# Optimization experiments

Hardware: AMD Instinct MI355X
Metric: run time of the kernel (lower is better)

Reference implementation:

```python
import jax, jax.numpy as jnp
import numpy as np

B, N = 8, 4096
DL = DR = DO = R = 256
SP = 3  # spatial tensor index dimension


def setup_inputs() -> dict:
    key = jax.random.key(0)
    k1, k2, k3, k4, k5 = jax.random.split(key, 5)
    x_l = jax.random.normal(k1, (B, N, DL, SP), dtype=jnp.float32)
    x_r = jax.random.normal(k2, (B, N, DR, SP), dtype=jnp.float32)
    # TensLinear self_init: normal with std = fan_in**-0.5
    W_l = jax.random.normal(k3, (R, DL), dtype=jnp.float32) * DL ** (-0.5)
    W_r = jax.random.normal(k4, (R, DR), dtype=jnp.float32) * DR ** (-0.5)
    W_o = jax.random.normal(k5, (DO, R), dtype=jnp.float32) * R ** (-0.5)
    return {"x_l": x_l, "x_r": x_r, "W_l": W_l, "W_r": W_r, "W_o": W_o}


def reference(x_l, x_r, W_l, W_r, W_o):
    # lin_l / lin_r: channel mixing into shared rank dim (tensor indices untouched)
    xl = jnp.einsum('OI,bnIi->bnOi', W_l, x_l)          # [B,N,R,3]
    xr = jnp.einsum('OI,bnIj->bnOj', W_r, x_r)          # [B,N,R,3]
    # inds_l=1, inds_r=1, inds_o=2 => contracts=0: outer product '...i,...j->...ij'
    xo = jnp.einsum('bnri,bnrj->bnrij', xl, xr)          # [B,N,R,3,3]
    # lin_o: mix rank -> dim_o
    return jnp.einsum('OI,bnIij->bnOij', W_o, xo)        # [B,N,DO,3,3]
```

## Files before the change

### kernel.cpp

```cpp
#include <hip/hip_runtime.h>

typedef short bf16x8 __attribute__((ext_vector_type(8)));
typedef float f32x4 __attribute__((ext_vector_type(4)));

__device__ inline unsigned short f2bf(float f) {
    union { float f; unsigned u; } v; v.f = f;
    unsigned u = v.u;
    u += 0x7fffu + ((u >> 16) & 1u);
    return (unsigned short)(u >> 16);
}

#define KPAD 264

__global__ void prep_weights(const float* __restrict__ wl,
                             const float* __restrict__ wr,
                             const float* __restrict__ wo,
                             unsigned short* __restrict__ wsw) {
    int idx = blockIdx.x * 256 + threadIdx.x;
    int w    = idx >> 16;
    int e    = idx & 65535;
    int jj   = e & 7;
    int lane = (e >> 3) & 63;
    int kmt  = e >> 9;
    int ks   = kmt & 7;
    int mt   = kmt >> 3;
    int row = mt * 16 + (lane & 15);
    int col = ks * 32 + (lane >> 4) * 8 + jj;
    const float* src = (w == 0) ? wl : (w == 1) ? wr : wo;
    wsw[idx] = f2bf(src[row * 256 + col]);
}

__global__ __launch_bounds__(512, 4) void fused_kernel(
    const float* __restrict__ xl_g, const float* __restrict__ xr_g,
    const unsigned short* __restrict__ wsw, float* __restrict__ out) {

    __shared__ __align__(16) unsigned short lds[38016];

    const int tid  = threadIdx.x;
    const int blk  = blockIdx.x;
    const int wave = tid >> 6;
    const int lane = tid & 63;
    const int q    = lane >> 4;
    const int l15  = lane & 15;

    const float* srcs[2] = { xl_g + (size_t)blk * 12288, xr_g + (size_t)blk * 12288 };
    for (int a = 0; a < 2; ++a) {
        const float4* s4 = (const float4*)srcs[a];
        unsigned short* dst = lds + a * 12672;
        #pragma unroll
        for (int it = 0; it < 6; ++it) {
            int g4 = it * 512 + tid;
            float4 v = s4[g4];
            int g = g4 * 4;
            int tok = g / 768;
            int m0 = g - tok * 768;
            float vv[4] = {v.x, v.y, v.z, v.w};
            #pragma unroll
            for (int e = 0; e < 4; ++e) {
                int mm = m0 + e;
                int I = mm / 3;
                int i = mm - I * 3;
                dst[(i * 16 + tok) * KPAD + I] = f2bf(vv[e]);
            }
        }
    }
    __syncthreads();

    const bf16x8* wlf = (const bf16x8*)(wsw);
    const bf16x8* wrf = (const bf16x8*)(wsw + 65536);
    const bf16x8* wof = (const bf16x8*)(wsw + 131072);

    f32x4 accL[2][3] = {};
    f32x4 accR[2][3] = {};

    #pragma unroll
    for (int k = 0; k < 8; ++k) {
        const int koff = k * 32 + q * 8;
        bf16x8 bl[3], br[3];
        #pragma unroll
        for (int nt = 0; nt < 3; ++nt) {
            bl[nt] = *(const bf16x8*)&lds[(nt * 16 + l15) * KPAD + koff];
            br[nt] = *(const bf16x8*)&lds[12672 + (nt * 16 + l15) * KPAD + koff];
        }
        #pragma unroll
        for (int m = 0; m < 2; ++m) {
            const int mt = wave * 2 + m;
            bf16x8 al = wlf[(mt * 8 + k) * 64 + lane];
            bf16x8 ar = wrf[(mt * 8 + k) * 64 + lane];
            #pragma unroll
            for (int nt = 0; nt < 3; ++nt) {
                accL[m][nt] = __builtin_amdgcn_mfma_f32_16x16x32_bf16(al, bl[nt], accL[m][nt], 0, 0, 0);
                accR[m][nt] = __builtin_amdgcn_mfma_f32_16x16x32_bf16(ar, br[nt], accR[m][nt], 0, 0, 0);
            }
        }
    }
    __syncthreads();

    #pragma unroll
    for (int m = 0; m < 2; ++m) {
        const int mt = wave * 2 + m;
        const int r0 = mt * 16 + q * 4;
        #pragma unroll
        for (int i = 0; i < 3; ++i) {
            #pragma unroll
            for (int j = 0; j < 3; ++j) {
                const int c = (i * 3 + j) * 16 + l15;
                unsigned short h[4];
                #pragma unroll
                for (int reg = 0; reg < 4; ++reg)
                    h[reg] = f2bf(accL[m][i][reg] * accR[m][j][reg]);
                uint2 pk;
                pk.x = (unsigned)h[0] | ((unsigned)h[1] << 16);
                pk.y = (unsigned)h[2] | ((unsigned)h[3] << 16);
                *(uint2*)&lds[c * KPAD + r0] = pk;
            }
        }
    }
    __syncthreads();

    const size_t tokbase = ((size_t)blk * 16 + l15) * 2304;
    #pragma unroll
    for (int pass = 0; pass < 2; ++pass) {
        const int p0 = pass ? 5 : 0;
        const int np = pass ? 4 : 5;
        f32x4 accO[2][5] = {};
        #pragma unroll
        for (int k = 0; k < 8; ++k) {
            const int koff = k * 32 + q * 8;
            bf16x8 pf[5];
            #pragma unroll
            for (int p = 0; p < np; ++p)
                pf[p] = *(const bf16x8*)&lds[((p0 + p) * 16 + l15) * KPAD + koff];
            #pragma unroll
            for (int m = 0; m < 2; ++m) {
                const int mt = wave * 2 + m;
                bf16x8 ao = wof[(mt * 8 + k) * 64 + lane];
                #pragma unroll
                for (int p = 0; p < np; ++p)
                    accO[m][p] = __builtin_amdgcn_mfma_f32_16x16x32_bf16(ao, pf[p], accO[m][p], 0, 0, 0);
            }
        }
        #pragma unroll
        for (int m = 0; m < 2; ++m) {
            const int mt = wave * 2 + m;
            #pragma unroll
            for (int reg = 0; reg < 4; ++reg) {
                const int o = mt * 16 + q * 4 + reg;
                float* dst = out + tokbase + o * 9 + p0;
                #pragma unroll
                for (int p = 0; p < np; ++p)
                    dst[p] = accO[m][p][reg];
            }
        }
    }
}

extern "C" void kernel_launch(void* const* d_in, const int* in_sizes, int n_in,
                              void* d_out, int out_size, void* d_ws, size_t ws_size,
                              hipStream_t stream) {
    const float* xl = (const float*)d_in[0];
    const float* xr = (const float*)d_in[1];
    const float* wl = (const float*)d_in[2];
    const float* wr = (const float*)d_in[3];
    const float* wo = (const float*)d_in[4];
    float* out = (float*)d_out;
    unsigned short* wsw = (unsigned short*)d_ws;

    prep_weights<<<768, 256, 0, stream>>>(wl, wr, wo, wsw);
    fused_kernel<<<2048, 512, 0, stream>>>(xl, xr, wsw, out);
}
```

Before: 534.1 us.

## Stage output tiles through LDS for coalesced float4 global stores

The final W_o GEMM now keeps both pass accumulators live and writes results into a per-wave LDS staging area, then writes contiguous float4 chunks per token to global memory. Previously each lane scattered scalar stores with a stride of 9 floats, which coalesces poorly for an output that dominates memory traffic. In exchange it raises register pressure, since all 9 accumulator tiles are live at once, and adds extra barriers and LDS traffic.

```diff
diff --git a/kernel.cpp b/kernel.cpp
--- a/kernel.cpp
+++ b/kernel.cpp
@@ -118,40 +118,65 @@
     }
     __syncthreads();
 
-    const size_t tokbase = ((size_t)blk * 16 + l15) * 2304;
+    f32x4 accA[2][5] = {};
+    f32x4 accB[2][4] = {};
     #pragma unroll
-    for (int pass = 0; pass < 2; ++pass) {
-        const int p0 = pass ? 5 : 0;
-        const int np = pass ? 4 : 5;
-        f32x4 accO[2][5] = {};
+    for (int k = 0; k < 8; ++k) {
+        const int koff = k * 32 + q * 8;
+        bf16x8 pf[5];
         #pragma unroll
-        for (int k = 0; k < 8; ++k) {
-            const int koff = k * 32 + q * 8;
-            bf16x8 pf[5];
-            #pragma unroll
-            for (int p = 0; p < np; ++p)
-                pf[p] = *(const bf16x8*)&lds[((p0 + p) * 16 + l15) * KPAD + koff];
-            #pragma unroll
-            for (int m = 0; m < 2; ++m) {
-                const int mt = wave * 2 + m;
-                bf16x8 ao = wof[(mt * 8 + k) * 64 + lane];
-                #pragma unroll
-                for (int p = 0; p < np; ++p)
-                    accO[m][p] = __builtin_amdgcn_mfma_f32_16x16x32_bf16(ao, pf[p], accO[m][p], 0, 0, 0);
-            }
-        }
+        for (int p = 0; p < 5; ++p)
+            pf[p] = *(const bf16x8*)&lds[(p * 16 + l15) * KPAD + koff];
         #pragma unroll
         for (int m = 0; m < 2; ++m) {
             const int mt = wave * 2 + m;
+            bf16x8 ao = wof[(mt * 8 + k) * 64 + lane];
             #pragma unroll
-            for (int reg = 0; reg < 4; ++reg) {
-                const int o = mt * 16 + q * 4 + reg;
-                float* dst = out + tokbase + o * 9 + p0;
-                #pragma unroll
-                for (int p = 0; p < np; ++p)
-                    dst[p] = accO[m][p][reg];
+            for (int p = 0; p < 5; ++p)
+                accA[m][p] = __builtin_amdgcn_mfma_f32_16x16x32_bf16(ao, pf[p], accA[m][p], 0, 0, 0);
+        }
+    }
+    #pragma unroll
+    for (int k = 0; k < 8; ++k) {
+        const int koff = k * 32 + q * 8;
+        bf16x8 pf[4];
+        #pragma unroll
+        for (int p = 0; p < 4; ++p)
+            pf[p] = *(const bf16x8*)&lds[((5 + p) * 16 + l15) * KPAD + koff];
+        #pragma unroll
+        for (int m = 0; m < 2; ++m) {
+            const int mt = wave * 2 + m;
+            bf16x8 ao = wof[(mt * 8 + k) * 64 + lane];
+            #pragma unroll
+            for (int p = 0; p < 4; ++p)
+                accB[m][p] = __builtin_amdgcn_mfma_f32_16x16x32_bf16(ao, pf[p], accB[m][p], 0, 0, 0);
+        }
+    }
+    __syncthreads();
+
+    float* sf = (float*)(lds + wave * 4736);
+    const int tok = lane >> 2, sub = lane & 3;
+    #pragma unroll
+    for (int m = 0; m < 2; ++m) {
+        const int mt = wave * 2 + m;
+        #pragma unroll
+        for (int reg = 0; reg < 4; ++reg) {
+            const int o9 = (q * 4 + reg) * 9;
+            #pragma unroll
+            for (int p = 0; p < 9; ++p) {
+                float v = (p < 5) ? accA[m][p][reg] : accB[m][p - 5][reg];
+                sf[l15 * 148 + o9 + p] = v;
             }
         }
+        __syncthreads();
+        float* wdst = out + ((size_t)blk * 16 + tok) * 2304 + mt * 144;
+        #pragma unroll
+        for (int it = 0; it < 9; ++it) {
+            const int f4 = sub + 4 * it;
+            float4 v = *(const float4*)&sf[tok * 148 + f4 * 4];
+            ((float4*)wdst)[f4] = v;
+        }
+        __syncthreads();
     }
 }
 
```

Result: faster. 486.3 us (-8.9%).
